# Kernel tuning notes

Measured on AMD Instinct MI355X. Metric: run time of the kernel, lower is better.

The kernel has to match this reference:

```python
import jax, jax.numpy as jnp
import numpy as np


def _sliding_window_attention(q, k, v, window_size, padding_mask):
    # q,k,v: [B,H,S,D]; faithful to the torch code incl. clamped scatter_add
    # duplicates at boundaries and the (score==0 -> -inf) quirk.
    B, H, S, D = q.shape
    hw = window_size // 2
    kp = jnp.pad(k, ((0, 0), (0, 0), (hw, hw), (0, 0)))  # zero-pad seq dim
    # window gather positions into padded keys: [S, W+1]
    pos = jnp.arange(S)[:, None] + jnp.arange(window_size + 1)[None, :]
    kw = kp[:, :, pos, :]  # [B,H,S,W+1,D]
    scores = jnp.einsum('bhsd,bhswd->bhsw', q, kw) / jnp.sqrt(jnp.asarray(D, q.dtype))
    # scatter-add into full [B,H,S,S] with clamped column indices (duplicates sum)
    idx = jnp.clip(jnp.arange(S)[:, None] + jnp.arange(-hw, hw + 1)[None, :], 0, S - 1)  # [S,W+1]
    rows = jnp.arange(S)[:, None]
    full = jnp.zeros((B, H, S, S), q.dtype).at[:, :, rows, idx].add(scores)
    neg_inf = jnp.asarray(-jnp.inf, full.dtype)
    full = jnp.where(full == 0.0, neg_inf, full)
    if padding_mask is not None:
        pm = padding_mask[:, None, None, :]  # [B,1,1,S]
        full = jnp.where(pm == 0, neg_inf, full)
        full = jnp.where(jnp.swapaxes(pm, -1, -2) == 0, neg_inf, full)
    att = jax.nn.softmax(full, axis=-1)
    att = jnp.where(jnp.isnan(att), jnp.asarray(0.0, att.dtype), att)
    values = jnp.einsum('bhst,bhtd->bhsd', att, v)
    return values, att


def setup_inputs() -> dict:
    key = jax.random.key(0)
    ks = jax.random.split(key, 5)
    B, S, IN_DIM, E = 2, 2048, 512, 512
    x = jax.random.normal(ks[0], (B, S, IN_DIM), dtype=jnp.float32)
    padding_mask = jnp.ones((B, S), dtype=jnp.int32)
    qkv_w = jax.random.normal(ks[1], (3 * E, IN_DIM), dtype=jnp.float32) * 0.02
    qkv_b = jnp.zeros((3 * E,), dtype=jnp.float32)
    o_w = jax.random.normal(ks[2], (E, E), dtype=jnp.float32) * 0.02
    o_b = jnp.zeros((E,), dtype=jnp.float32)
    return {'x': x, 'padding_mask': padding_mask, 'qkv_w': qkv_w, 'qkv_b': qkv_b,
            'o_w': o_w, 'o_b': o_b, 'window_size': 256, 'num_heads': 8}


def reference(x, padding_mask, qkv_w, qkv_b, o_w, o_b, window_size, num_heads):
    B, S, _ = x.shape
    E3 = qkv_w.shape[0]
    E = E3 // 3
    head_dim = E // num_heads
    qkv = x @ qkv_w.T + qkv_b                         # [B,S,3E]
    qkv = qkv.reshape(B, S, num_heads, 3 * head_dim)
    qkv = jnp.transpose(qkv, (0, 2, 1, 3))            # [B,H,S,3*hd]
    q, k, v = jnp.split(qkv, 3, axis=-1)
    values, _ = _sliding_window_attention(q, k, v, window_size, padding_mask)
    values = jnp.transpose(values, (0, 2, 1, 3)).reshape(B, S, E)
    o = values @ o_w.T + o_b
    return o
```

## Files before the change

kernel.cpp:

```cpp
#include <hip/hip_runtime.h>
#include <hip/hip_bf16.h>
#include <math.h>


typedef __bf16 bf16x8 __attribute__((ext_vector_type(8)));
typedef float f32x4 __attribute__((ext_vector_type(4)));

__device__ __forceinline__ unsigned short f2bf(float f) {
  unsigned u = __float_as_uint(f);
  unsigned r = u + 0x7FFFu + ((u >> 16) & 1u);
  return (unsigned short)(r >> 16);
}

__device__ __forceinline__ void ldsdma16(void* lds, const void* g) {
  __builtin_amdgcn_global_load_lds(
      (const __attribute__((address_space(1))) unsigned int*)g,
      (__attribute__((address_space(3))) unsigned int*)lds, 16, 0, 0);
}

__global__ __launch_bounds__(256) void cvt3_kernel(
    const float* __restrict__ s0, unsigned short* __restrict__ d0, int n0,
    const float* __restrict__ s1, unsigned short* __restrict__ d1, int n1,
    const float* __restrict__ s2, unsigned short* __restrict__ d2, int n2) {
  int i4 = blockIdx.x * 256 + threadIdx.x;
  const int c0 = n0 >> 2, c1 = (n0 + n1) >> 2, c2 = (n0 + n1 + n2) >> 2;
  const float* s; unsigned short* d; int base4;
  if (i4 < c0)      { s = s0; d = d0; base4 = i4; }
  else if (i4 < c1) { s = s1; d = d1; base4 = i4 - c0; }
  else if (i4 < c2) { s = s2; d = d2; base4 = i4 - c1; }
  else return;
  float4 v = ((const float4*)s)[base4];
  ushort4 o;
  o.x = f2bf(v.x); o.y = f2bf(v.y); o.z = f2bf(v.z); o.w = f2bf(v.w);
  ((ushort4*)d)[base4] = o;
}

__global__ __launch_bounds__(256) void gemm_qkv(
    const __hip_bfloat16* __restrict__ A, const __hip_bfloat16* __restrict__ Bw,
    const float* __restrict__ bias,
    __hip_bfloat16* __restrict__ qp, __hip_bfloat16* __restrict__ kpb,
    unsigned short* __restrict__ vtb) {
  __shared__ __hip_bfloat16 As[128 * 32];
  __shared__ __hip_bfloat16 Bs[128 * 32];

  const int tid = threadIdx.x, wave = tid >> 6, lane = tid & 63;
  const int m0 = blockIdx.x * 128, n0 = blockIdx.y * 128;
  const int wm = (wave >> 1) * 64, wn = (wave & 1) * 64;
  const int cl = lane & 15, ko = (lane >> 4) * 8;
  const int srow = wave * 16 + (lane >> 2);
  const int scol = (lane & 3) * 8;

  f32x4 acc[4][4] = {};

  for (int k0 = 0; k0 < 512; k0 += 32) {
    __syncthreads();
    ldsdma16(&As[wave * 512],        A  + (size_t)(m0 + srow) * 512 + k0 + scol);
    ldsdma16(&As[2048 + wave * 512], A  + (size_t)(m0 + 64 + srow) * 512 + k0 + scol);
    ldsdma16(&Bs[wave * 512],        Bw + (size_t)(n0 + srow) * 512 + k0 + scol);
    ldsdma16(&Bs[2048 + wave * 512], Bw + (size_t)(n0 + 64 + srow) * 512 + k0 + scol);
    __syncthreads();

    bf16x8 af[4], bf[4];
#pragma unroll
    for (int i = 0; i < 4; i++)
      af[i] = *(const bf16x8*)(&As[(wm + cl + i * 16) * 32 + ko]);
#pragma unroll
    for (int i = 0; i < 4; i++)
      bf[i] = *(const bf16x8*)(&Bs[(wn + cl + i * 16) * 32 + ko]);
#pragma unroll
    for (int mi = 0; mi < 4; mi++)
#pragma unroll
      for (int ni = 0; ni < 4; ni++)
        acc[mi][ni] = __builtin_amdgcn_mfma_f32_16x16x32_bf16(
            af[mi], bf[ni], acc[mi][ni], 0, 0, 0);
  }

  const int crow = (lane >> 4) * 4;
#pragma unroll
  for (int mi = 0; mi < 4; mi++) {
    const int mb = m0 + wm + mi * 16 + crow;
    const int bq = mb >> 11, sl = mb & 2047;
#pragma unroll
    for (int ni = 0; ni < 4; ni++) {
      const int n = n0 + wn + ni * 16 + cl;
      const int h = n / 192;
      const int rem = n - h * 192;
      const int cat = rem >> 6;
      const int d = rem & 63;
      const float bv = bias[n];
      const size_t bh = (size_t)bq * 8 + h;
      if (cat == 2) {
        ushort4 o;
        o.x = f2bf(acc[mi][ni][0] + bv);
        o.y = f2bf(acc[mi][ni][1] + bv);
        o.z = f2bf(acc[mi][ni][2] + bv);
        o.w = f2bf(acc[mi][ni][3] + bv);
        *(ushort4*)(vtb + (bh * 64 + d) * 2048 + sl) = o;
      } else {
        __hip_bfloat16* dst = (cat == 0) ? qp : kpb;
        const float sc = (cat == 0) ? 0.18033688011112042f : 1.0f;
#pragma unroll
        for (int r = 0; r < 4; r++)
          dst[(bh * 2048 + sl + r) * 64 + d] =
              __float2bfloat16((acc[mi][ni][r] + bv) * sc);
      }
    }
  }
}

__global__ __launch_bounds__(256) void attn_mfma(
    const __hip_bfloat16* __restrict__ qp, const __hip_bfloat16* __restrict__ kp,
    const __hip_bfloat16* __restrict__ vt, const int* __restrict__ pm,
    __hip_bfloat16* __restrict__ vals) {
  __shared__ __hip_bfloat16 sKP[320 * 72];
  __shared__ float sCM[320];

  const int tid = threadIdx.x, wave = tid >> 6, lane = tid & 63;
  const int bid = blockIdx.x;
  const int s0 = (bid & 31) * 64;
  const int bh = bid >> 5;
  const int b = bh >> 3, h = bh & 7;
  const int t0 = s0 - 128;
  const int cl = lane & 15;
  const int g4 = (lane >> 4) * 4;
  const int ko = (lane >> 4) * 8;

  {
    const int e = (tid & 7) * 8;
#pragma unroll
    for (int i = 0; i < 10; i++) {
      int row = (tid >> 3) + i * 32;
      int t = t0 + row; t = min(max(t, 0), 2047);
      *(uint4*)(&sKP[row * 72 + e]) =
          *(const uint4*)(kp + ((size_t)bh * 2048 + t) * 64 + e);
    }
  }
  for (int c = tid; c < 320; c += 256) {
    int t = t0 + c;
    bool ok = (t >= 0 && t < 2048) && (pm[b * 2048 + t] != 0);
    sCM[c] = ok ? 0.0f : -3.0e38f;
  }
  __syncthreads();

  const __hip_bfloat16* qrow =
      qp + ((size_t)bh * 2048 + s0 + wave * 16 + cl) * 64 + ko;
  bf16x8 aq0 = *(const bf16x8*)(qrow);
  bf16x8 aq1 = *(const bf16x8*)(qrow + 32);

  f32x4 acc[17];
#pragma unroll
  for (int i = 0; i < 17; i++) {
    const int krow = (wave + i) * 16 + cl;
    bf16x8 b0 = *(const bf16x8*)(&sKP[krow * 72 + ko]);
    bf16x8 b1 = *(const bf16x8*)(&sKP[krow * 72 + ko + 32]);
    f32x4 z = {};
    z = __builtin_amdgcn_mfma_f32_16x16x32_bf16(aq0, b0, z, 0, 0, 0);
    acc[i] = __builtin_amdgcn_mfma_f32_16x16x32_bf16(aq1, b1, z, 0, 0, 0);
  }

  float mrow[4] = {-3.0e38f, -3.0e38f, -3.0e38f, -3.0e38f};
#pragma unroll
  for (int i = 0; i < 17; i++) {
    const float ca = sCM[(wave + i) * 16 + cl];
#pragma unroll
    for (int r = 0; r < 4; r++) {
      float sv = acc[i][r] + ca;
      if (i == 0) {
        if (cl < g4 + r) sv = -3.0e38f;
      } else if (i == 16) {
        if (cl > g4 + r) sv = -3.0e38f;
      }
      acc[i][r] = sv;
      mrow[r] = fmaxf(mrow[r], sv);
    }
  }
#pragma unroll
  for (int r = 0; r < 4; r++)
#pragma unroll
    for (int off = 1; off < 16; off <<= 1)
      mrow[r] = fmaxf(mrow[r], __shfl_xor(mrow[r], off));

  float lsum[4] = {0.f, 0.f, 0.f, 0.f};
#pragma unroll
  for (int i = 0; i < 17; i++)
#pragma unroll
    for (int r = 0; r < 4; r++) {
      float p = exp2f(acc[i][r] - mrow[r]);
      acc[i][r] = p;
      lsum[r] += p;
    }
#pragma unroll
  for (int r = 0; r < 4; r++)
#pragma unroll
    for (int off = 1; off < 16; off <<= 1)
      lsum[r] += __shfl_xor(lsum[r], off);

  __syncthreads();

  __hip_bfloat16* sp = sKP + wave * 5248;
#pragma unroll
  for (int i = 0; i < 17; i++) {
    const int c = (wave + i) * 16 + cl;
#pragma unroll
    for (int r = 0; r < 4; r++)
      sp[(g4 + r) * 328 + c] = __float2bfloat16(acc[i][r]);
  }
  {
    const int zt = (wave & 1) ? (wave - 1) : (wave + 17);
    const int zc = zt * 16 + cl;
#pragma unroll
    for (int r = 0; r < 4; r++)
      sp[(g4 + r) * 328 + zc] = __float2bfloat16(0.f);
  }
  __syncthreads();

  f32x4 oacc[4] = {};
  const int k0 = wave >> 1;
  const __hip_bfloat16* vbase = vt + (size_t)bh * 64 * 2048;
#pragma unroll
  for (int ks = 0; ks < 9; ks++) {
    const int kk = (k0 + ks) * 32 + ko;
    bf16x8 pa = *(const bf16x8*)(&sp[cl * 328 + kk]);
    int tv = t0 + kk; tv = min(max(tv, 0), 2040);
#pragma unroll
    for (int ni = 0; ni < 4; ni++) {
      const int d = ni * 16 + cl;
      bf16x8 vb = *(const bf16x8*)(vbase + (size_t)d * 2048 + tv);
      oacc[ni] = __builtin_amdgcn_mfma_f32_16x16x32_bf16(pa, vb, oacc[ni], 0, 0, 0);
    }
  }

#pragma unroll
  for (int r = 0; r < 4; r++) {
    float linv = 1.0f / fmaxf(lsum[r], 1e-20f);
    const int qr = wave * 16 + g4 + r;
    if (sCM[qr + 128] != 0.0f) linv = 0.0f;
    const size_t obase = ((size_t)(b * 2048 + s0 + qr)) * 512 + h * 64 + cl;
#pragma unroll
    for (int ni = 0; ni < 4; ni++)
      vals[obase + ni * 16] = __float2bfloat16(oacc[ni][r] * linv);
  }
}

__global__ __launch_bounds__(256) void gemm_out(
    const __hip_bfloat16* __restrict__ A, const __hip_bfloat16* __restrict__ Bw,
    const float* __restrict__ bias, float* __restrict__ C) {
  __shared__ __hip_bfloat16 As[64 * 32];
  __shared__ __hip_bfloat16 Bs[128 * 32];

  const int tid = threadIdx.x, wave = tid >> 6, lane = tid & 63;
  const int m0 = blockIdx.x * 64, n0 = blockIdx.y * 128;
  const int wm = (wave >> 1) * 32, wn = (wave & 1) * 64;
  const int cl = lane & 15, ko = (lane >> 4) * 8;
  const int srow = wave * 16 + (lane >> 2);
  const int scol = (lane & 3) * 8;

  f32x4 acc[2][4] = {};

  for (int k0 = 0; k0 < 512; k0 += 32) {
    __syncthreads();
    ldsdma16(&As[wave * 512],        A  + (size_t)(m0 + srow) * 512 + k0 + scol);
    ldsdma16(&Bs[wave * 512],        Bw + (size_t)(n0 + srow) * 512 + k0 + scol);
    ldsdma16(&Bs[2048 + wave * 512], Bw + (size_t)(n0 + 64 + srow) * 512 + k0 + scol);
    __syncthreads();

    bf16x8 af[2], bf[4];
#pragma unroll
    for (int i = 0; i < 2; i++)
      af[i] = *(const bf16x8*)(&As[(wm + cl + i * 16) * 32 + ko]);
#pragma unroll
    for (int i = 0; i < 4; i++)
      bf[i] = *(const bf16x8*)(&Bs[(wn + cl + i * 16) * 32 + ko]);
#pragma unroll
    for (int mi = 0; mi < 2; mi++)
#pragma unroll
      for (int ni = 0; ni < 4; ni++)
        acc[mi][ni] = __builtin_amdgcn_mfma_f32_16x16x32_bf16(
            af[mi], bf[ni], acc[mi][ni], 0, 0, 0);
  }

  const int crow = (lane >> 4) * 4;
#pragma unroll
  for (int mi = 0; mi < 2; mi++) {
#pragma unroll
    for (int ni = 0; ni < 4; ni++) {
      const int n = n0 + wn + ni * 16 + cl;
      const float bv = bias[n];
      const int mb = m0 + wm + mi * 16 + crow;
#pragma unroll
      for (int r = 0; r < 4; r++)
        C[(size_t)(mb + r) * 512 + n] = acc[mi][ni][r] + bv;
    }
  }
}

extern "C" void kernel_launch(void* const* d_in, const int* in_sizes, int n_in,
                              void* d_out, int out_size, void* d_ws, size_t ws_size,
                              hipStream_t stream) {
  const float* x     = (const float*)d_in[0];
  const int*   pm    = (const int*)d_in[1];
  const float* qkv_w = (const float*)d_in[2];
  const float* qkv_b = (const float*)d_in[3];
  const float* o_w   = (const float*)d_in[4];
  const float* o_b   = (const float*)d_in[5];
  float* out = (float*)d_out;

  __hip_bfloat16* wsb   = (__hip_bfloat16*)d_ws;
  __hip_bfloat16* xb    = wsb;
  __hip_bfloat16* wqkvb = wsb + 2097152;
  __hip_bfloat16* wob   = wsb + 2883584;
  __hip_bfloat16* qp    = wsb + 3145728;
  __hip_bfloat16* kp    = wsb + 5242880;
  __hip_bfloat16* vt    = wsb + 7340032;
  __hip_bfloat16* vals  = wsb + 9437184;

  dim3 blk(256);
  cvt3_kernel<<<dim3(3072), blk, 0, stream>>>(
      x, (unsigned short*)xb, 2097152,
      qkv_w, (unsigned short*)wqkvb, 786432,
      o_w, (unsigned short*)wob, 262144);
  gemm_qkv<<<dim3(32, 12), blk, 0, stream>>>(
      xb, wqkvb, qkv_b, qp, kp, (unsigned short*)vt);
  attn_mfma<<<dim3(512), blk, 0, stream>>>(qp, kp, vt, pm, vals);
  gemm_out<<<dim3(64, 4), blk, 0, stream>>>(vals, wob, o_b, out);
}
```

Before: 118.9 us.

## Halve QKV GEMM M-tile and load attention keys directly from global memory

The QKV projection GEMM tile drops from 128x128 to 64x128 and the grid doubles to 768 blocks, so more of the GPU's compute units get work. The attention kernel no longer stages the 320-row key window in shared memory; each wave reads its key fragments straight from global memory, and the probability buffer becomes a private per-wave region, which removes two block-wide barriers. This trades shared-memory reuse of keys for redundant global/L2 reads across waves, and the GEMM gets less reuse of B per block.

```diff
diff --git a/kernel.cpp b/kernel.cpp
--- a/kernel.cpp
+++ b/kernel.cpp
@@ -40,35 +40,34 @@
     const float* __restrict__ bias,
     __hip_bfloat16* __restrict__ qp, __hip_bfloat16* __restrict__ kpb,
     unsigned short* __restrict__ vtb) {
-  __shared__ __hip_bfloat16 As[128 * 32];
+  __shared__ __hip_bfloat16 As[64 * 32];
   __shared__ __hip_bfloat16 Bs[128 * 32];
 
   const int tid = threadIdx.x, wave = tid >> 6, lane = tid & 63;
-  const int m0 = blockIdx.x * 128, n0 = blockIdx.y * 128;
-  const int wm = (wave >> 1) * 64, wn = (wave & 1) * 64;
+  const int m0 = blockIdx.x * 64, n0 = blockIdx.y * 128;
+  const int wm = (wave >> 1) * 32, wn = (wave & 1) * 64;
   const int cl = lane & 15, ko = (lane >> 4) * 8;
   const int srow = wave * 16 + (lane >> 2);
   const int scol = (lane & 3) * 8;
 
-  f32x4 acc[4][4] = {};
+  f32x4 acc[2][4] = {};
 
   for (int k0 = 0; k0 < 512; k0 += 32) {
     __syncthreads();
     ldsdma16(&As[wave * 512],        A  + (size_t)(m0 + srow) * 512 + k0 + scol);
-    ldsdma16(&As[2048 + wave * 512], A  + (size_t)(m0 + 64 + srow) * 512 + k0 + scol);
     ldsdma16(&Bs[wave * 512],        Bw + (size_t)(n0 + srow) * 512 + k0 + scol);
     ldsdma16(&Bs[2048 + wave * 512], Bw + (size_t)(n0 + 64 + srow) * 512 + k0 + scol);
     __syncthreads();
 
-    bf16x8 af[4], bf[4];
-#pragma unroll
-    for (int i = 0; i < 4; i++)
+    bf16x8 af[2], bf[4];
+#pragma unroll
+    for (int i = 0; i < 2; i++)
       af[i] = *(const bf16x8*)(&As[(wm + cl + i * 16) * 32 + ko]);
 #pragma unroll
     for (int i = 0; i < 4; i++)
       bf[i] = *(const bf16x8*)(&Bs[(wn + cl + i * 16) * 32 + ko]);
 #pragma unroll
-    for (int mi = 0; mi < 4; mi++)
+    for (int mi = 0; mi < 2; mi++)
 #pragma unroll
       for (int ni = 0; ni < 4; ni++)
         acc[mi][ni] = __builtin_amdgcn_mfma_f32_16x16x32_bf16(
@@ -77,7 +76,7 @@
 
   const int crow = (lane >> 4) * 4;
 #pragma unroll
-  for (int mi = 0; mi < 4; mi++) {
+  for (int mi = 0; mi < 2; mi++) {
     const int mb = m0 + wm + mi * 16 + crow;
     const int bq = mb >> 11, sl = mb & 2047;
 #pragma unroll
@@ -112,7 +111,7 @@
     const __hip_bfloat16* __restrict__ qp, const __hip_bfloat16* __restrict__ kp,
     const __hip_bfloat16* __restrict__ vt, const int* __restrict__ pm,
     __hip_bfloat16* __restrict__ vals) {
-  __shared__ __hip_bfloat16 sKP[320 * 72];
+  __shared__ __hip_bfloat16 sP[4 * 16 * 296];
   __shared__ float sCM[320];
 
   const int tid = threadIdx.x, wave = tid >> 6, lane = tid & 63;
@@ -125,16 +124,6 @@
   const int g4 = (lane >> 4) * 4;
   const int ko = (lane >> 4) * 8;
 
-  {
-    const int e = (tid & 7) * 8;
-#pragma unroll
-    for (int i = 0; i < 10; i++) {
-      int row = (tid >> 3) + i * 32;
-      int t = t0 + row; t = min(max(t, 0), 2047);
-      *(uint4*)(&sKP[row * 72 + e]) =
-          *(const uint4*)(kp + ((size_t)bh * 2048 + t) * 64 + e);
-    }
-  }
   for (int c = tid; c < 320; c += 256) {
     int t = t0 + c;
     bool ok = (t >= 0 && t < 2048) && (pm[b * 2048 + t] != 0);
@@ -147,12 +136,15 @@
   bf16x8 aq0 = *(const bf16x8*)(qrow);
   bf16x8 aq1 = *(const bf16x8*)(qrow + 32);
 
+  const __hip_bfloat16* kbase = kp + (size_t)bh * 2048 * 64;
   f32x4 acc[17];
 #pragma unroll
   for (int i = 0; i < 17; i++) {
-    const int krow = (wave + i) * 16 + cl;
-    bf16x8 b0 = *(const bf16x8*)(&sKP[krow * 72 + ko]);
-    bf16x8 b1 = *(const bf16x8*)(&sKP[krow * 72 + ko + 32]);
+    int t = t0 + (wave + i) * 16 + cl;
+    t = min(max(t, 0), 2047);
+    const __hip_bfloat16* kr = kbase + (size_t)t * 64 + ko;
+    bf16x8 b0 = *(const bf16x8*)(kr);
+    bf16x8 b1 = *(const bf16x8*)(kr + 32);
     f32x4 z = {};
     z = __builtin_amdgcn_mfma_f32_16x16x32_bf16(aq0, b0, z, 0, 0, 0);
     acc[i] = __builtin_amdgcn_mfma_f32_16x16x32_bf16(aq1, b1, z, 0, 0, 0);
@@ -195,33 +187,30 @@
     for (int off = 1; off < 16; off <<= 1)
       lsum[r] += __shfl_xor(lsum[r], off);
 
-  __syncthreads();
-
-  __hip_bfloat16* sp = sKP + wave * 5248;
+  __hip_bfloat16* sp = sP + wave * (16 * 296);
+  const int roff = (wave & 1) << 4;
 #pragma unroll
   for (int i = 0; i < 17; i++) {
-    const int c = (wave + i) * 16 + cl;
+    const int rel = i * 16 + cl + roff;
 #pragma unroll
     for (int r = 0; r < 4; r++)
-      sp[(g4 + r) * 328 + c] = __float2bfloat16(acc[i][r]);
+      sp[(g4 + r) * 296 + rel] = __float2bfloat16(acc[i][r]);
   }
   {
-    const int zt = (wave & 1) ? (wave - 1) : (wave + 17);
-    const int zc = zt * 16 + cl;
+    const int zc = (wave & 1) ? cl : (272 + cl);
 #pragma unroll
     for (int r = 0; r < 4; r++)
-      sp[(g4 + r) * 328 + zc] = __float2bfloat16(0.f);
-  }
-  __syncthreads();
+      sp[(g4 + r) * 296 + zc] = __float2bfloat16(0.f);
+  }
 
   f32x4 oacc[4] = {};
-  const int k0 = wave >> 1;
+  const int kb0 = (wave >> 1) * 32;
   const __hip_bfloat16* vbase = vt + (size_t)bh * 64 * 2048;
 #pragma unroll
   for (int ks = 0; ks < 9; ks++) {
-    const int kk = (k0 + ks) * 32 + ko;
-    bf16x8 pa = *(const bf16x8*)(&sp[cl * 328 + kk]);
-    int tv = t0 + kk; tv = min(max(tv, 0), 2040);
+    const int rel = ks * 32 + ko;
+    bf16x8 pa = *(const bf16x8*)(&sp[cl * 296 + rel]);
+    int tv = t0 + kb0 + rel; tv = min(max(tv, 0), 2040);
 #pragma unroll
     for (int ni = 0; ni < 4; ni++) {
       const int d = ni * 16 + cl;
@@ -319,7 +308,7 @@
       x, (unsigned short*)xb, 2097152,
       qkv_w, (unsigned short*)wqkvb, 786432,
       o_w, (unsigned short*)wob, 262144);
-  gemm_qkv<<<dim3(32, 12), blk, 0, stream>>>(
+  gemm_qkv<<<dim3(64, 12), blk, 0, stream>>>(
       xb, wqkvb, qkv_b, qp, kp, (unsigned short*)vt);
   attn_mfma<<<dim3(512), blk, 0, stream>>>(qp, kp, vt, pm, vals);
   gemm_out<<<dim3(64, 4), blk, 0, stream>>>(vals, wob, o_b, out);
```

Measured after the change: 126.9 us. 6.8% more time.
